# Kernel tuning notes

Measured on AMD Instinct MI355X. Metric: run time of the kernel, lower is better.

## Reference

```python
import jax, jax.numpy as jnp
import numpy as np

N = 50000   # num_nodes
E = 600000  # num_edges (avg degree 12)
D = 128     # feats_dim


def setup_inputs() -> dict:
    key = jax.random.key(0)
    ks = jax.random.split(key, 10)
    s = 1.0 / np.sqrt(D)
    return {
        "node_ids": jnp.arange(N, dtype=jnp.int32),
        "edge_src": jax.random.randint(ks[0], (E,), 0, N, dtype=jnp.int32),
        "edge_dst": jax.random.randint(ks[1], (E,), 0, N, dtype=jnp.int32),
        "edge_weight": jax.random.uniform(ks[2], (E,), dtype=jnp.float32),
        "emb": jax.random.normal(ks[3], (N, D), dtype=jnp.float32),
        "W_self1": jax.random.uniform(ks[4], (D, D), jnp.float32, -s, s),
        "W_neigh1": jax.random.uniform(ks[5], (D, D), jnp.float32, -s, s),
        "b1": jnp.zeros((D,), jnp.float32),
        "W_self2": jax.random.uniform(ks[6], (D, D), jnp.float32, -s, s),
        "W_neigh2": jax.random.uniform(ks[7], (D, D), jnp.float32, -s, s),
        "b2": jnp.zeros((D,), jnp.float32),
    }


def _sage_conv(h, src, dst, w, W_self, W_neigh, b):
    # DGL SAGEConv('mean') with edge_weight: neigh = mean_in(w_e * h_src)
    msg = h[src] * w[:, None]                                  # [E, D] gather
    neigh_sum = jax.ops.segment_sum(msg, dst, num_segments=N)  # [N, D] scatter-add
    deg = jax.ops.segment_sum(jnp.ones_like(w), dst, num_segments=N)
    neigh = neigh_sum / jnp.maximum(deg, 1.0)[:, None]         # 0 for isolated nodes
    # fc_self carries the bias, fc_neigh has none (DGL convention)
    return h @ W_self.T + b + neigh @ W_neigh.T


def reference(node_ids, edge_src, edge_dst, edge_weight, emb,
              W_self1, W_neigh1, b1, W_self2, W_neigh2, b2):
    h = emb[node_ids]                                          # embedding lookup
    h = _sage_conv(h, edge_src, edge_dst, edge_weight, W_self1, W_neigh1, b1)
    h = jax.nn.relu(h)
    h = _sage_conv(h, edge_src, edge_dst, edge_weight, W_self2, W_neigh2, b2)
    return h
```

## Files before the change

kernel.cpp:

```cpp
#include <hip/hip_runtime.h>
#include <stdint.h>

#define DIM 128

typedef __attribute__((ext_vector_type(8))) short bf16x8;
typedef __attribute__((ext_vector_type(4))) float floatx4;

__device__ __forceinline__ float bf2f(unsigned short u) {
    union { unsigned int i; float f; } v; v.i = ((unsigned int)u) << 16; return v.f;
}
__device__ __forceinline__ unsigned short f2bf(float f) {
    union { float f; unsigned int i; } v; v.f = f;
    unsigned int r = (v.i + 0x7FFFu + ((v.i >> 16) & 1u)) >> 16;
    return (unsigned short)r;
}

__device__ __forceinline__ int block_flag(const unsigned int* __restrict__ emb32) {
    __shared__ int sf;
    if (threadIdx.x < 64) {
        unsigned int v = emb32[threadIdx.x];
        float f = bf2f((unsigned short)(v & 0xffffu));
        int bad = !(fabsf(f) < 1e4f);
        unsigned long long m = __ballot(bad);
        if (threadIdx.x == 0) sf = (__popcll(m) > 16) ? 1 : 0;
    }
    __syncthreads();
    return sf;
}


__global__ __launch_bounds__(256) void bucket_hist(const int* __restrict__ dst,
                                                   int* __restrict__ bcnt, int E, int NB) {
    __shared__ int cnt[256];
    int t = threadIdx.x, j = blockIdx.x;
    cnt[t] = 0;
    __syncthreads();
    int chunk = (E + 255) / 256;
    int beg = j * chunk;
    int end = min(beg + chunk, E);
    for (int e = beg + t; e < end; e += 256) atomicAdd(&cnt[(dst[e] >> 8) & 255], 1);
    __syncthreads();
    if (t < NB) bcnt[j * NB + t] = cnt[t];
}

__global__ __launch_bounds__(256) void bucket_scan(const int* __restrict__ bcnt,
                                                   int* __restrict__ boff,
                                                   int* __restrict__ btot, int NB) {
    __shared__ int tile[256];
    int t = threadIdx.x, k = blockIdx.x;
    int v = bcnt[t * NB + k];
    tile[t] = v;
    __syncthreads();
    for (int off = 1; off < 256; off <<= 1) {
        int x = (t >= off) ? tile[t - off] : 0;
        __syncthreads();
        tile[t] += x;
        __syncthreads();
    }
    boff[t * NB + k] = tile[t] - v;
    if (t == 255) btot[k] = tile[255];
}

__global__ __launch_bounds__(256) void bucket_scatter(
        const int* __restrict__ src, const int* __restrict__ dst,
        const void* __restrict__ w_any, const unsigned int* __restrict__ emb32,
        const int* __restrict__ boff, const int* __restrict__ btot,
        unsigned int* __restrict__ s_tmp, unsigned char* __restrict__ s_tmpb,
        int E, int NB) {
    int flag = block_flag(emb32);
    __shared__ int bs[256];
    __shared__ int cursor[256];
    int t = threadIdx.x, j = blockIdx.x;
    int bv = (t < NB) ? btot[t] : 0;
    bs[t] = bv;
    __syncthreads();
    for (int off = 1; off < 256; off <<= 1) {
        int x = (t >= off) ? bs[t - off] : 0;
        __syncthreads();
        bs[t] += x;
        __syncthreads();
    }
    cursor[t] = (bs[t] - bv) + ((t < NB) ? boff[j * NB + t] : 0);
    __syncthreads();
    int chunk = (E + 255) / 256;
    int beg = j * chunk;
    int end = min(beg + chunk, E);
    for (int e = beg + t; e < end; e += 256) {
        int d = dst[e];
        unsigned short wb = flag ? f2bf(((const float*)w_any)[e])
                                 : ((const unsigned short*)w_any)[e];
        unsigned int rec = ((unsigned int)src[e] & 0xffffu) | ((unsigned int)wb << 16);
        int pos = atomicAdd(&cursor[(d >> 8) & 255], 1);
        s_tmp[pos] = rec;
        s_tmpb[pos] = (unsigned char)(d & 255);
    }
}

__global__ __launch_bounds__(256) void bucket_csr(
        const int* __restrict__ btot,
        const unsigned int* __restrict__ s_tmp, const unsigned char* __restrict__ s_tmpb,
        unsigned int* __restrict__ s_edge, int* __restrict__ row_ptr, int N, int NB) {
    __shared__ int bs[256];
    __shared__ int hist[256];
    __shared__ int cur[256];
    int t = threadIdx.x, b = blockIdx.x;
    int bv = (t < NB) ? btot[t] : 0;
    bs[t] = bv;
    __syncthreads();
    for (int off = 1; off < 256; off <<= 1) {
        int x = (t >= off) ? bs[t - off] : 0;
        __syncthreads();
        bs[t] += x;
        __syncthreads();
    }
    int myEnd = bs[b];
    int myStart = myEnd - btot[b];
    hist[t] = 0;
    __syncthreads();
    for (int e = myStart + t; e < myEnd; e += 256) atomicAdd(&hist[s_tmpb[e]], 1);
    __syncthreads();
    int hv = hist[t];
    for (int off = 1; off < 256; off <<= 1) {
        int x = (t >= off) ? hist[t - off] : 0;
        __syncthreads();
        hist[t] += x;
        __syncthreads();
    }
    int rowstart = myStart + hist[t] - hv;
    int node = b * 256 + t;
    if (node < N) row_ptr[node] = rowstart;
    if (b == NB - 1 && t == 0) row_ptr[N] = myEnd;
    cur[t] = rowstart;
    __syncthreads();
    for (int e = myStart + t; e < myEnd; e += 256) {
        unsigned int rec = s_tmp[e];
        int pos = atomicAdd(&cur[s_tmpb[e]], 1);
        s_edge[pos] = rec;
    }
}

__global__ __launch_bounds__(256) void prep_kernel(
        const void* __restrict__ s0, const void* __restrict__ s1,
        const void* __restrict__ s2, const void* __restrict__ s3,
        const void* __restrict__ s4, const void* __restrict__ s5,
        unsigned short* __restrict__ wcat,
        const int* __restrict__ ids, const void* __restrict__ emb,
        unsigned int* __restrict__ h032,
        int conv_blocks, int total_gather) {
    int flag = block_flag((const unsigned int*)emb);
    const int W = DIM * DIM;
    int blk = (int)blockIdx.x;
    if (blk < conv_blocks) {
        int i = blk * 256 + threadIdx.x;
        const void* srcp; int off;
        if      (i < W)             { srcp = s0; off = i; }
        else if (i < 2 * W)         { srcp = s1; off = i - W; }
        else if (i < 3 * W)         { srcp = s2; off = i - 2 * W; }
        else if (i < 4 * W)         { srcp = s3; off = i - 3 * W; }
        else if (i < 4 * W + DIM)   { srcp = s4; off = i - 4 * W; }
        else if (i < 4 * W + 2*DIM) { srcp = s5; off = i - 4 * W - DIM; }
        else return;
        wcat[i] = flag ? f2bf(((const float*)srcp)[off])
                       : ((const unsigned short*)srcp)[off];
    } else {
        int t = (blk - conv_blocks) * 256 + threadIdx.x;
        if (t >= total_gather) return;
        int n = t >> 6;
        int f = t & 63;
        int id = ids[n];
        unsigned int o;
        if (flag) {
            const float* e = (const float*)emb + (size_t)id * DIM + f * 2;
            o = ((unsigned int)f2bf(e[1]) << 16) | (unsigned int)f2bf(e[0]);
        } else {
            o = ((const unsigned int*)emb)[(size_t)id * 64 + f];
        }
        h032[t] = o;
    }
}


__global__ __launch_bounds__(256) void agg_kernel(const uint2* __restrict__ h64,
                                                  const int* __restrict__ row_ptr,
                                                  const unsigned int* __restrict__ s_edge,
                                                  uint2* __restrict__ out64,
                                                  int N, int E) {
    int lane = threadIdx.x & 63;
    int half = lane >> 5;
    int sub  = lane & 31;
    int node = blockIdx.x * 8 + (threadIdx.x >> 6) * 2 + half;
    if (node >= N) return;
    int beg = max(row_ptr[node], 0);
    int end = min(row_ptr[node + 1], E);
    float a0 = 0.f, a1 = 0.f, a2 = 0.f, a3 = 0.f;
    int e = beg;
    for (; e + 8 <= end; e += 8) {
        unsigned int r[8]; int k[8]; float w[8]; uint2 v[8];
#pragma unroll
        for (int i = 0; i < 8; ++i) r[i] = s_edge[e + i];
#pragma unroll
        for (int i = 0; i < 8; ++i) {
            k[i] = min((int)(r[i] & 0xffffu), N - 1);
            w[i] = bf2f((unsigned short)(r[i] >> 16));
        }
#pragma unroll
        for (int i = 0; i < 8; ++i) v[i] = h64[(size_t)k[i] * 32 + sub];
#pragma unroll
        for (int i = 0; i < 8; ++i) {
            a0 += w[i] * bf2f((unsigned short)(v[i].x & 0xffffu));
            a1 += w[i] * bf2f((unsigned short)(v[i].x >> 16));
            a2 += w[i] * bf2f((unsigned short)(v[i].y & 0xffffu));
            a3 += w[i] * bf2f((unsigned short)(v[i].y >> 16));
        }
    }
    for (; e + 4 <= end; e += 4) {
        unsigned int r[4]; int k[4]; float w[4]; uint2 v[4];
#pragma unroll
        for (int i = 0; i < 4; ++i) r[i] = s_edge[e + i];
#pragma unroll
        for (int i = 0; i < 4; ++i) {
            k[i] = min((int)(r[i] & 0xffffu), N - 1);
            w[i] = bf2f((unsigned short)(r[i] >> 16));
        }
#pragma unroll
        for (int i = 0; i < 4; ++i) v[i] = h64[(size_t)k[i] * 32 + sub];
#pragma unroll
        for (int i = 0; i < 4; ++i) {
            a0 += w[i] * bf2f((unsigned short)(v[i].x & 0xffffu));
            a1 += w[i] * bf2f((unsigned short)(v[i].x >> 16));
            a2 += w[i] * bf2f((unsigned short)(v[i].y & 0xffffu));
            a3 += w[i] * bf2f((unsigned short)(v[i].y >> 16));
        }
    }
    for (; e < end; ++e) {
        unsigned int r = s_edge[e];
        int k = min((int)(r & 0xffffu), N - 1);
        float w = bf2f((unsigned short)(r >> 16));
        uint2 v = h64[(size_t)k * 32 + sub];
        a0 += w * bf2f((unsigned short)(v.x & 0xffffu));
        a1 += w * bf2f((unsigned short)(v.x >> 16));
        a2 += w * bf2f((unsigned short)(v.y & 0xffffu));
        a3 += w * bf2f((unsigned short)(v.y >> 16));
    }
    float inv = (end > beg) ? 1.0f / (float)(end - beg) : 0.f;
    a0 *= inv; a1 *= inv; a2 *= inv; a3 *= inv;
    uint2 o;
    o.x = ((unsigned int)f2bf(a1) << 16) | (unsigned int)f2bf(a0);
    o.y = ((unsigned int)f2bf(a3) << 16) | (unsigned int)f2bf(a2);
    out64[(size_t)node * 32 + sub] = o;
}


#define WROW 68

__global__ __launch_bounds__(256) void gemm_layer(const unsigned short* __restrict__ A0,
                                                  const unsigned short* __restrict__ A1,
                                                  const unsigned short* __restrict__ W0,
                                                  const unsigned short* __restrict__ W1,
                                                  const unsigned short* __restrict__ bias,
                                                  void* __restrict__ out,
                                                  const unsigned int* __restrict__ emb32,
                                                  int n_rows, int relu, int is_final) {
    __shared__ unsigned int lw[2 * DIM * WROW];
    int fp32_out = is_final ? block_flag(emb32) : (void(block_flag(emb32)), 0);
    int t = threadIdx.x;

#pragma unroll
    for (int mat = 0; mat < 2; ++mat) {
        const uint4* src = (const uint4*)(mat ? W1 : W0);
        unsigned int* dstl = lw + mat * DIM * WROW;
#pragma unroll
        for (int i = 0; i < 8; ++i) {
            int c = i * 256 + t;
            uint4 v = src[c];
            *(uint4*)&dstl[(c >> 4) * WROW + (c & 15) * 4] = v;
        }
    }
    __syncthreads();

    int wave = t >> 6;
    int lane = t & 63;
    int quad = lane >> 4;
    int l16  = lane & 15;
    int m_base = blockIdx.x * 128 + wave * 32;

    floatx4 acc0[8], acc1[8];
#pragma unroll
    for (int c = 0; c < 8; ++c) {
        acc0[c] = (floatx4){0.f, 0.f, 0.f, 0.f};
        acc1[c] = (floatx4){0.f, 0.f, 0.f, 0.f};
    }

    int r0 = min(m_base + l16, n_rows - 1);
    int r1 = min(m_base + 16 + l16, n_rows - 1);

#pragma unroll
    for (int mat = 0; mat < 2; ++mat) {
        const unsigned short* A  = mat ? A1 : A0;
        const unsigned int* lwm = lw + mat * DIM * WROW;
        const unsigned short* Ar0 = A + (size_t)r0 * DIM;
        const unsigned short* Ar1 = A + (size_t)r1 * DIM;
#pragma unroll
        for (int ks = 0; ks < 4; ++ks) {
            int k0 = ks * 32 + quad * 8;
            bf16x8 a0 = *(const bf16x8*)(Ar0 + k0);
            bf16x8 a1 = *(const bf16x8*)(Ar1 + k0);
#pragma unroll
            for (int c = 0; c < 8; ++c) {
                bf16x8 b = *(const bf16x8*)&lwm[(c * 16 + l16) * WROW + (k0 >> 1)];
                acc0[c] = __builtin_amdgcn_mfma_f32_16x16x32_bf16(a0, b, acc0[c], 0, 0, 0);
                acc1[c] = __builtin_amdgcn_mfma_f32_16x16x32_bf16(a1, b, acc1[c], 0, 0, 0);
            }
        }
    }

#pragma unroll
    for (int c = 0; c < 8; ++c) {
        int col = c * 16 + l16;
        float bv = bf2f(bias[col]);
#pragma unroll
        for (int r = 0; r < 4; ++r) {
            int row0 = m_base + quad * 4 + r;
            int row1 = row0 + 16;
            if (row0 < n_rows) {
                float v = acc0[c][r] + bv;
                if (relu) v = fmaxf(v, 0.f);
                size_t idx = (size_t)row0 * DIM + col;
                if (fp32_out) ((float*)out)[idx] = v;
                else          ((unsigned short*)out)[idx] = f2bf(v);
            }
            if (row1 < n_rows) {
                float v = acc1[c][r] + bv;
                if (relu) v = fmaxf(v, 0.f);
                size_t idx = (size_t)row1 * DIM + col;
                if (fp32_out) ((float*)out)[idx] = v;
                else          ((unsigned short*)out)[idx] = f2bf(v);
            }
        }
    }
}


extern "C" void kernel_launch(void* const* d_in, const int* in_sizes, int n_in,
                              void* d_out, int out_size, void* d_ws, size_t ws_size,
                              hipStream_t stream) {
    const int* node_ids = (const int*)d_in[0];
    const int* edge_src = (const int*)d_in[1];
    const int* edge_dst = (const int*)d_in[2];
    const void* edge_w  = d_in[3];
    const void* emb     = d_in[4];
    const void* Ws1     = d_in[5];
    const void* Wn1     = d_in[6];
    const void* b1      = d_in[7];
    const void* Ws2     = d_in[8];
    const void* Wn2     = d_in[9];
    const void* b2      = d_in[10];

    const int N = in_sizes[0];
    const int E = in_sizes[1];
    const int NB = (N + 255) >> 8;

    char* w = (char*)d_ws;
    auto alloc = [&](size_t bytes) {
        char* p = w;
        w += (bytes + 255) & ~(size_t)255;
        return p;
    };
    int* bcnt           = (int*)alloc((size_t)256 * NB * 4);
    int* boff           = (int*)alloc((size_t)256 * NB * 4);
    int* btot           = (int*)alloc((size_t)256 * 4);
    int* row_ptr        = (int*)alloc((size_t)(N + 1) * 4);
    const int W = DIM * DIM;
    unsigned short* wcat = (unsigned short*)alloc((size_t)(4 * W + 2 * DIM) * 2);
    unsigned short* Ws1c = wcat;
    unsigned short* Wn1c = wcat + W;
    unsigned short* Ws2c = wcat + 2 * W;
    unsigned short* Wn2c = wcat + 3 * W;
    unsigned short* b1c  = wcat + 4 * W;
    unsigned short* b2c  = wcat + 4 * W + DIM;
    unsigned int* s_tmp  = (unsigned int*)alloc((size_t)E * 4);
    unsigned char* s_tmpb = (unsigned char*)alloc((size_t)E);
    unsigned int* s_edge = (unsigned int*)alloc((size_t)E * 4);
    unsigned short* h0  = (unsigned short*)alloc((size_t)N * DIM * 2);
    unsigned short* h1  = (unsigned short*)alloc((size_t)N * DIM * 2);
    unsigned short* ngh = (unsigned short*)alloc((size_t)N * DIM * 2);

    const unsigned int* emb32 = (const unsigned int*)emb;

    bucket_hist<<<256, 256, 0, stream>>>(edge_dst, bcnt, E, NB);
    bucket_scan<<<NB, 256, 0, stream>>>(bcnt, boff, btot, NB);
    bucket_scatter<<<256, 256, 0, stream>>>(edge_src, edge_dst, edge_w, emb32,
                                            boff, btot, s_tmp, s_tmpb, E, NB);
    bucket_csr<<<NB, 256, 0, stream>>>(btot, s_tmp, s_tmpb, s_edge, row_ptr, N, NB);

    const int CN = 4 * W + 2 * DIM;
    const int conv_blocks = (CN + 255) / 256;
    const int gather_total = N * 64;
    const int gather_blocks = (gather_total + 255) / 256;
    prep_kernel<<<conv_blocks + gather_blocks, 256, 0, stream>>>(
        Ws1, Wn1, Ws2, Wn2, b1, b2, wcat, node_ids, emb,
        (unsigned int*)h0, conv_blocks, gather_total);

    agg_kernel<<<(N + 7) / 8, 256, 0, stream>>>((const uint2*)h0, row_ptr,
                                                s_edge, (uint2*)ngh, N, E);
    gemm_layer<<<(N + 127) / 128, 256, 0, stream>>>(h0, ngh, Ws1c, Wn1c, b1c,
                                                    h1, emb32, N, 1, 0);

    agg_kernel<<<(N + 7) / 8, 256, 0, stream>>>((const uint2*)h1, row_ptr,
                                                s_edge, (uint2*)ngh, N, E);
    gemm_layer<<<(N + 127) / 128, 256, 0, stream>>>(h1, ngh, Ws2c, Wn2c, b2c,
                                                    d_out, emb32, N, 0, 1);
}
```

Before: 215.2 us.

## Widen aggregation loads to 16-byte vectors and fuse histogram with prep kernel

The aggregation kernel now has 16 lanes per node, each loading a uint4 (8 bf16 values) instead of 32 lanes loading uint2. Each block now covers 16 nodes. This cuts the number of gather instructions and raises memory-level parallelism per wavefront, at the cost of more registers per thread. The bucket histogram and the weight/embedding prep kernel are merged into one launch, removing one kernel launch and letting the independent work overlap.

```diff
diff --git a/kernel.cpp b/kernel.cpp
--- a/kernel.cpp
+++ b/kernel.cpp
@@ -13,6 +13,9 @@
     union { float f; unsigned int i; } v; v.f = f;
     unsigned int r = (v.i + 0x7FFFu + ((v.i >> 16) & 1u)) >> 16;
     return (unsigned short)r;
+}
+__device__ __forceinline__ unsigned int pack2(float lo, float hi) {
+    return ((unsigned int)f2bf(hi) << 16) | (unsigned int)f2bf(lo);
 }
 
 __device__ __forceinline__ int block_flag(const unsigned int* __restrict__ emb32) {
@@ -28,19 +31,57 @@
     return sf;
 }
 
-
-__global__ __launch_bounds__(256) void bucket_hist(const int* __restrict__ dst,
-                                                   int* __restrict__ bcnt, int E, int NB) {
-    __shared__ int cnt[256];
-    int t = threadIdx.x, j = blockIdx.x;
-    cnt[t] = 0;
-    __syncthreads();
-    int chunk = (E + 255) / 256;
-    int beg = j * chunk;
-    int end = min(beg + chunk, E);
-    for (int e = beg + t; e < end; e += 256) atomicAdd(&cnt[(dst[e] >> 8) & 255], 1);
-    __syncthreads();
-    if (t < NB) bcnt[j * NB + t] = cnt[t];
+__global__ __launch_bounds__(256) void hist_prep_kernel(
+        const int* __restrict__ dst, int* __restrict__ bcnt, int E, int NB,
+        const void* __restrict__ s0, const void* __restrict__ s1,
+        const void* __restrict__ s2, const void* __restrict__ s3,
+        const void* __restrict__ s4, const void* __restrict__ s5,
+        unsigned short* __restrict__ wcat,
+        const int* __restrict__ ids, const void* __restrict__ emb,
+        unsigned int* __restrict__ h032,
+        int conv_blocks, int total_gather) {
+    const int W = DIM * DIM;
+    int blk = (int)blockIdx.x;
+    int t = threadIdx.x;
+    if (blk < 256) {
+        __shared__ int cnt[256];
+        cnt[t] = 0;
+        __syncthreads();
+        int chunk = (E + 255) / 256;
+        int beg = blk * chunk;
+        int end = min(beg + chunk, E);
+        for (int e = beg + t; e < end; e += 256) atomicAdd(&cnt[(dst[e] >> 8) & 255], 1);
+        __syncthreads();
+        if (t < NB) bcnt[blk * NB + t] = cnt[t];
+    } else if (blk < 256 + conv_blocks) {
+        int flag = block_flag((const unsigned int*)emb);
+        int i = (blk - 256) * 256 + t;
+        const void* srcp; int off;
+        if      (i < W)             { srcp = s0; off = i; }
+        else if (i < 2 * W)         { srcp = s1; off = i - W; }
+        else if (i < 3 * W)         { srcp = s2; off = i - 2 * W; }
+        else if (i < 4 * W)         { srcp = s3; off = i - 3 * W; }
+        else if (i < 4 * W + DIM)   { srcp = s4; off = i - 4 * W; }
+        else if (i < 4 * W + 2*DIM) { srcp = s5; off = i - 4 * W - DIM; }
+        else return;
+        wcat[i] = flag ? f2bf(((const float*)srcp)[off])
+                       : ((const unsigned short*)srcp)[off];
+    } else {
+        int flag = block_flag((const unsigned int*)emb);
+        int g = (blk - 256 - conv_blocks) * 256 + t;
+        if (g >= total_gather) return;
+        int n = g >> 6;
+        int f = g & 63;
+        int id = ids[n];
+        unsigned int o;
+        if (flag) {
+            const float* e = (const float*)emb + (size_t)id * DIM + f * 2;
+            o = (pack2(e[0], e[1]));
+        } else {
+            o = ((const unsigned int*)emb)[(size_t)id * 64 + f];
+        }
+        h032[g] = o;
+    }
 }
 
 __global__ __launch_bounds__(256) void bucket_scan(const int* __restrict__ bcnt,
@@ -139,63 +180,24 @@
     }
 }
 
-__global__ __launch_bounds__(256) void prep_kernel(
-        const void* __restrict__ s0, const void* __restrict__ s1,
-        const void* __restrict__ s2, const void* __restrict__ s3,
-        const void* __restrict__ s4, const void* __restrict__ s5,
-        unsigned short* __restrict__ wcat,
-        const int* __restrict__ ids, const void* __restrict__ emb,
-        unsigned int* __restrict__ h032,
-        int conv_blocks, int total_gather) {
-    int flag = block_flag((const unsigned int*)emb);
-    const int W = DIM * DIM;
-    int blk = (int)blockIdx.x;
-    if (blk < conv_blocks) {
-        int i = blk * 256 + threadIdx.x;
-        const void* srcp; int off;
-        if      (i < W)             { srcp = s0; off = i; }
-        else if (i < 2 * W)         { srcp = s1; off = i - W; }
-        else if (i < 3 * W)         { srcp = s2; off = i - 2 * W; }
-        else if (i < 4 * W)         { srcp = s3; off = i - 3 * W; }
-        else if (i < 4 * W + DIM)   { srcp = s4; off = i - 4 * W; }
-        else if (i < 4 * W + 2*DIM) { srcp = s5; off = i - 4 * W - DIM; }
-        else return;
-        wcat[i] = flag ? f2bf(((const float*)srcp)[off])
-                       : ((const unsigned short*)srcp)[off];
-    } else {
-        int t = (blk - conv_blocks) * 256 + threadIdx.x;
-        if (t >= total_gather) return;
-        int n = t >> 6;
-        int f = t & 63;
-        int id = ids[n];
-        unsigned int o;
-        if (flag) {
-            const float* e = (const float*)emb + (size_t)id * DIM + f * 2;
-            o = ((unsigned int)f2bf(e[1]) << 16) | (unsigned int)f2bf(e[0]);
-        } else {
-            o = ((const unsigned int*)emb)[(size_t)id * 64 + f];
-        }
-        h032[t] = o;
-    }
-}
-
-
-__global__ __launch_bounds__(256) void agg_kernel(const uint2* __restrict__ h64,
+
+__global__ __launch_bounds__(256) void agg_kernel(const uint4* __restrict__ h128,
                                                   const int* __restrict__ row_ptr,
                                                   const unsigned int* __restrict__ s_edge,
-                                                  uint2* __restrict__ out64,
+                                                  uint4* __restrict__ out128,
                                                   int N, int E) {
     int lane = threadIdx.x & 63;
-    int half = lane >> 5;
-    int sub  = lane & 31;
-    int node = blockIdx.x * 8 + (threadIdx.x >> 6) * 2 + half;
+    int q    = lane >> 4;
+    int sub  = lane & 15;
+    int node = blockIdx.x * 16 + (threadIdx.x >> 6) * 4 + q;
     if (node >= N) return;
     int beg = max(row_ptr[node], 0);
     int end = min(row_ptr[node + 1], E);
     float a0 = 0.f, a1 = 0.f, a2 = 0.f, a3 = 0.f;
+    float a4 = 0.f, a5 = 0.f, a6 = 0.f, a7 = 0.f;
     int e = beg;
     for (; e + 8 <= end; e += 8) {
-        unsigned int r[8]; int k[8]; float w[8]; uint2 v[8];
+        unsigned int r[8]; int k[8]; float w[8]; uint4 v[8];
 #pragma unroll
         for (int i = 0; i < 8; ++i) r[i] = s_edge[e + i];
 #pragma unroll
@@ -204,17 +206,21 @@
             w[i] = bf2f((unsigned short)(r[i] >> 16));
         }
 #pragma unroll
-        for (int i = 0; i < 8; ++i) v[i] = h64[(size_t)k[i] * 32 + sub];
+        for (int i = 0; i < 8; ++i) v[i] = h128[(size_t)k[i] * 16 + sub];
 #pragma unroll
         for (int i = 0; i < 8; ++i) {
             a0 += w[i] * bf2f((unsigned short)(v[i].x & 0xffffu));
             a1 += w[i] * bf2f((unsigned short)(v[i].x >> 16));
             a2 += w[i] * bf2f((unsigned short)(v[i].y & 0xffffu));
             a3 += w[i] * bf2f((unsigned short)(v[i].y >> 16));
+            a4 += w[i] * bf2f((unsigned short)(v[i].z & 0xffffu));
+            a5 += w[i] * bf2f((unsigned short)(v[i].z >> 16));
+            a6 += w[i] * bf2f((unsigned short)(v[i].w & 0xffffu));
+            a7 += w[i] * bf2f((unsigned short)(v[i].w >> 16));
         }
     }
     for (; e + 4 <= end; e += 4) {
-        unsigned int r[4]; int k[4]; float w[4]; uint2 v[4];
+        unsigned int r[4]; int k[4]; float w[4]; uint4 v[4];
 #pragma unroll
         for (int i = 0; i < 4; ++i) r[i] = s_edge[e + i];
 #pragma unroll
@@ -223,31 +229,40 @@
             w[i] = bf2f((unsigned short)(r[i] >> 16));
         }
 #pragma unroll
-        for (int i = 0; i < 4; ++i) v[i] = h64[(size_t)k[i] * 32 + sub];
+        for (int i = 0; i < 4; ++i) v[i] = h128[(size_t)k[i] * 16 + sub];
 #pragma unroll
         for (int i = 0; i < 4; ++i) {
             a0 += w[i] * bf2f((unsigned short)(v[i].x & 0xffffu));
             a1 += w[i] * bf2f((unsigned short)(v[i].x >> 16));
             a2 += w[i] * bf2f((unsigned short)(v[i].y & 0xffffu));
             a3 += w[i] * bf2f((unsigned short)(v[i].y >> 16));
+            a4 += w[i] * bf2f((unsigned short)(v[i].z & 0xffffu));
+            a5 += w[i] * bf2f((unsigned short)(v[i].z >> 16));
+            a6 += w[i] * bf2f((unsigned short)(v[i].w & 0xffffu));
+            a7 += w[i] * bf2f((unsigned short)(v[i].w >> 16));
         }
     }
     for (; e < end; ++e) {
         unsigned int r = s_edge[e];
         int k = min((int)(r & 0xffffu), N - 1);
         float w = bf2f((unsigned short)(r >> 16));
-        uint2 v = h64[(size_t)k * 32 + sub];
+        uint4 v = h128[(size_t)k * 16 + sub];
         a0 += w * bf2f((unsigned short)(v.x & 0xffffu));
         a1 += w * bf2f((unsigned short)(v.x >> 16));
         a2 += w * bf2f((unsigned short)(v.y & 0xffffu));
         a3 += w * bf2f((unsigned short)(v.y >> 16));
+        a4 += w * bf2f((unsigned short)(v.z & 0xffffu));
+        a5 += w * bf2f((unsigned short)(v.z >> 16));
+        a6 += w * bf2f((unsigned short)(v.w & 0xffffu));
+        a7 += w * bf2f((unsigned short)(v.w >> 16));
     }
     float inv = (end > beg) ? 1.0f / (float)(end - beg) : 0.f;
-    a0 *= inv; a1 *= inv; a2 *= inv; a3 *= inv;
-    uint2 o;
-    o.x = ((unsigned int)f2bf(a1) << 16) | (unsigned int)f2bf(a0);
-    o.y = ((unsigned int)f2bf(a3) << 16) | (unsigned int)f2bf(a2);
-    out64[(size_t)node * 32 + sub] = o;
+    uint4 o;
+    o.x = pack2(a0 * inv, a1 * inv);
+    o.y = pack2(a2 * inv, a3 * inv);
+    o.z = pack2(a4 * inv, a5 * inv);
+    o.w = pack2(a6 * inv, a7 * inv);
+    out128[(size_t)node * 16 + sub] = o;
 }
 
 
@@ -387,27 +402,27 @@
 
     const unsigned int* emb32 = (const unsigned int*)emb;
 
-    bucket_hist<<<256, 256, 0, stream>>>(edge_dst, bcnt, E, NB);
+    const int CN = 4 * W + 2 * DIM;
+    const int conv_blocks = (CN + 255) / 256;
+    const int gather_total = N * 64;
+    const int gather_blocks = (gather_total + 255) / 256;
+
+    hist_prep_kernel<<<256 + conv_blocks + gather_blocks, 256, 0, stream>>>(
+        edge_dst, bcnt, E, NB,
+        Ws1, Wn1, Ws2, Wn2, b1, b2, wcat, node_ids, emb,
+        (unsigned int*)h0, conv_blocks, gather_total);
     bucket_scan<<<NB, 256, 0, stream>>>(bcnt, boff, btot, NB);
     bucket_scatter<<<256, 256, 0, stream>>>(edge_src, edge_dst, edge_w, emb32,
                                             boff, btot, s_tmp, s_tmpb, E, NB);
     bucket_csr<<<NB, 256, 0, stream>>>(btot, s_tmp, s_tmpb, s_edge, row_ptr, N, NB);
 
-    const int CN = 4 * W + 2 * DIM;
-    const int conv_blocks = (CN + 255) / 256;
-    const int gather_total = N * 64;
-    const int gather_blocks = (gather_total + 255) / 256;
-    prep_kernel<<<conv_blocks + gather_blocks, 256, 0, stream>>>(
-        Ws1, Wn1, Ws2, Wn2, b1, b2, wcat, node_ids, emb,
-        (unsigned int*)h0, conv_blocks, gather_total);
-
-    agg_kernel<<<(N + 7) / 8, 256, 0, stream>>>((const uint2*)h0, row_ptr,
-                                                s_edge, (uint2*)ngh, N, E);
+    agg_kernel<<<(N + 15) / 16, 256, 0, stream>>>((const uint4*)h0, row_ptr,
+                                                  s_edge, (uint4*)ngh, N, E);
     gemm_layer<<<(N + 127) / 128, 256, 0, stream>>>(h0, ngh, Ws1c, Wn1c, b1c,
                                                     h1, emb32, N, 1, 0);
 
-    agg_kernel<<<(N + 7) / 8, 256, 0, stream>>>((const uint2*)h1, row_ptr,
-                                                s_edge, (uint2*)ngh, N, E);
+    agg_kernel<<<(N + 15) / 16, 256, 0, stream>>>((const uint4*)h1, row_ptr,
+                                                  s_edge, (uint4*)ngh, N, E);
     gemm_layer<<<(N + 127) / 128, 256, 0, stream>>>(h1, ngh, Ws2c, Wn2c, b2c,
                                                     d_out, emb32, N, 0, 1);
 }
```

Measured after the change: 211.5 us. About the same (-1.7%).
